# Performance work log

Measured on AMD Instinct MI355X. Metric: run time of the kernel, lower is better.

## Reference

```python
import jax, jax.numpy as jnp
import numpy as np

NUM_HEADS = 16
NUM_KV_HEADS = 8
HEAD_DIM = 256
HIDDEN = 2048
ROT_DIM = 64          # head_dim * partial_rotary_factor (0.25)
RMS_EPS = 1e-6
ROPE_THETA = 10000.0
SEQ = 2048


def _rmsnorm(x, weight=None):
    # Gemma RMSNorm: x * rsqrt(mean(x^2)+eps) * (1 + w); v_norm has no scale.
    var = jnp.mean(jnp.square(x), axis=-1, keepdims=True)
    n = x * jax.lax.rsqrt(var + RMS_EPS)
    if weight is not None:
        n = n * (1.0 + weight)
    return n


def _rope(x, positions):
    # Partial neox-style RoPE on the first ROT_DIM dims of each head.
    # x: [S, H, D]
    rot, rest = x[..., :ROT_DIM], x[..., ROT_DIM:]
    half = ROT_DIM // 2
    inv_freq = 1.0 / (ROPE_THETA ** (jnp.arange(0, ROT_DIM, 2, dtype=jnp.float32) / ROT_DIM))
    freqs = positions.astype(jnp.float32)[:, None] * inv_freq  # [S, half]
    cos = jnp.cos(freqs)[:, None, :]  # [S, 1, half]
    sin = jnp.sin(freqs)[:, None, :]
    x1, x2 = rot[..., :half], rot[..., half:]
    rot_out = jnp.concatenate([x1 * cos - x2 * sin, x2 * cos + x1 * sin], axis=-1)
    return jnp.concatenate([rot_out, rest], axis=-1)


def setup_inputs() -> dict:
    key = jax.random.key(0)
    k1, k2, k3, k4, k5 = jax.random.split(key, 5)
    q_size = NUM_HEADS * HEAD_DIM
    kv_size = NUM_KV_HEADS * HEAD_DIM
    return {
        "positions": jnp.arange(SEQ, dtype=jnp.int32),
        "hidden_states": jax.random.normal(k1, (SEQ, HIDDEN), dtype=jnp.float32),
        "w_qkv": jax.random.normal(k2, (q_size + 2 * kv_size, HIDDEN), dtype=jnp.float32) * (HIDDEN ** -0.5),
        "q_norm_w": jax.random.normal(k3, (HEAD_DIM,), dtype=jnp.float32) * 0.02,
        "k_norm_w": jax.random.normal(k4, (HEAD_DIM,), dtype=jnp.float32) * 0.02,
        "w_o": jax.random.normal(k5, (HIDDEN, q_size), dtype=jnp.float32) * (q_size ** -0.5),
    }


def reference(positions, hidden_states, w_qkv, q_norm_w, k_norm_w, w_o):
    S = hidden_states.shape[0]
    q_size = NUM_HEADS * HEAD_DIM
    kv_size = NUM_KV_HEADS * HEAD_DIM

    qkv = hidden_states @ w_qkv.T  # [S, q+2kv]
    q, k, v = jnp.split(qkv, [q_size, q_size + kv_size], axis=-1)
    q = q.reshape(S, NUM_HEADS, HEAD_DIM)
    k = k.reshape(S, NUM_KV_HEADS, HEAD_DIM)
    v = v.reshape(S, NUM_KV_HEADS, HEAD_DIM)

    # per-head RMSNorms (v_norm: scale_shift=0, with_scale=False -> pure norm)
    q = _rmsnorm(q, q_norm_w)
    k = _rmsnorm(k, k_norm_w)
    v = _rmsnorm(v, None)

    q = _rope(q, positions)
    k = _rope(k, positions)

    # GQA: repeat kv heads to match query heads
    rep = NUM_HEADS // NUM_KV_HEADS
    k = jnp.repeat(k, rep, axis=1)  # [S, H, D]
    v = jnp.repeat(v, rep, axis=1)

    # RadixAttention constructed with scaling=1.0 -> no 1/sqrt(d) scale
    scores = jnp.einsum("qhd,khd->hqk", q, k)  # [H, S, S]
    causal = positions[:, None] >= positions[None, :]  # [S, S]
    scores = jnp.where(causal[None, :, :], scores, jnp.float32(-1e30))
    attn = jax.nn.softmax(scores, axis=-1)
    out = jnp.einsum("hqk,khd->qhd", attn, v)  # [S, H, D]
    out = out.reshape(S, q_size)
    return out @ w_o.T  # [S, HIDDEN]
```

## Files before the change

kernel.cpp:

```cpp
#include <hip/hip_runtime.h>
#include <stdint.h>
#include <math.h>

#define SEQ 2048
#define HID 2048
#define NH 16
#define NKV 8
#define HD 256
#define QSZ 4096
#define QKVN 8192

typedef __attribute__((ext_vector_type(4))) float f32x4;
typedef _Float16 f16x8 __attribute__((ext_vector_type(8)));
typedef unsigned short u16;

__device__ __forceinline__ u16 f2h(float f) {
  _Float16 h = (_Float16)f;
  return __builtin_bit_cast(u16, h);
}
__device__ __forceinline__ float h2f(u16 b) {
  return (float)__builtin_bit_cast(_Float16, b);
}
__device__ __forceinline__ void glds16(const void* g, void* l) {
  __builtin_amdgcn_global_load_lds(
      (const __attribute__((address_space(1))) uint32_t*)g,
      (__attribute__((address_space(3))) uint32_t*)l, 16, 0, 0);
}

__global__ void cvt_f32_f16(const float* __restrict__ in, u16* __restrict__ out, int n4) {
  int i = blockIdx.x * 256 + threadIdx.x;
  if (i < n4) {
    float4 v = reinterpret_cast<const float4*>(in)[i];
    ushort4 o = make_ushort4(f2h(v.x), f2h(v.y), f2h(v.z), f2h(v.w));
    reinterpret_cast<ushort4*>(out)[i] = o;
  }
}

template <int F16OUT>
__global__ __launch_bounds__(256, 2) void gemm_bt(
    const u16* __restrict__ A, const u16* __restrict__ B, void* __restrict__ Cv,
    int M, int N, int K) {
  __shared__ __align__(16) u16 As[128 * 32];
  __shared__ __align__(16) u16 Bs[128 * 32];
  const int t = threadIdx.x;
  const int w = t >> 6, l = t & 63;
  const int bm = blockIdx.y * 128, bn = blockIdx.x * 128;
  const int wr = (w >> 1) * 64, wc = (w & 1) * 64;
  f32x4 acc[4][4] = {};

  const int arow = t >> 2;
  const int acol = (t & 3) * 8;
  const u16* Ag0 = A + (size_t)(bm + arow) * K + acol;
  const u16* Ag1 = A + (size_t)(bm + 64 + arow) * K + acol;
  const u16* Bg0 = B + (size_t)(bn + arow) * K + acol;
  const u16* Bg1 = B + (size_t)(bn + 64 + arow) * K + acol;
  u16* Al0 = As + w * 512;
  u16* Al1 = As + 2048 + w * 512;
  u16* Bl0 = Bs + w * 512;
  u16* Bl1 = Bs + 2048 + w * 512;

  const int lr = l & 15;
  const int lko = (l >> 4) * 8;

  for (int k0 = 0; k0 < K; k0 += 32) {
    __syncthreads();
    glds16(Ag0 + k0, Al0);
    glds16(Ag1 + k0, Al1);
    glds16(Bg0 + k0, Bl0);
    glds16(Bg1 + k0, Bl1);
    __syncthreads();
    f16x8 a[4], b[4];
#pragma unroll
    for (int m = 0; m < 4; ++m) a[m] = *(const f16x8*)&As[(wr + m * 16 + lr) * 32 + lko];
#pragma unroll
    for (int n = 0; n < 4; ++n) b[n] = *(const f16x8*)&Bs[(wc + n * 16 + lr) * 32 + lko];
#pragma unroll
    for (int m = 0; m < 4; ++m)
#pragma unroll
      for (int n = 0; n < 4; ++n)
        acc[m][n] = __builtin_amdgcn_mfma_f32_16x16x32_f16(a[m], b[n], acc[m][n], 0, 0, 0);
  }

#pragma unroll
  for (int m = 0; m < 4; ++m) {
#pragma unroll
    for (int n = 0; n < 4; ++n) {
      const int col = bn + wc + n * 16 + lr;
      const int row0 = bm + wr + m * 16 + (l >> 4) * 4;
#pragma unroll
      for (int j = 0; j < 4; ++j) {
        float vv = acc[m][n][j];
        if constexpr (F16OUT)
          ((u16*)Cv)[(size_t)(row0 + j) * N + col] = f2h(vv);
        else
          ((float*)Cv)[(size_t)(row0 + j) * N + col] = vv;
      }
    }
  }
}

__global__ void norm_rope(const u16* __restrict__ qkv, const float* __restrict__ qw,
                          const float* __restrict__ kw, const int* __restrict__ pos,
                          u16* __restrict__ qo, u16* __restrict__ ko, u16* __restrict__ vt) {
  const int b = blockIdx.x;
  const int s = b >> 5;
  const int slot = b & 31;
  const int l = threadIdx.x;
  const u16* row = qkv + (size_t)s * QKVN + slot * HD;
  ushort4 rv = *reinterpret_cast<const ushort4*>(row + l * 4);
  float x0 = h2f(rv.x), x1 = h2f(rv.y), x2 = h2f(rv.z), x3 = h2f(rv.w);
  float ss = x0 * x0 + x1 * x1 + x2 * x2 + x3 * x3;
#pragma unroll
  for (int mk = 32; mk; mk >>= 1) ss += __shfl_xor(ss, mk);
  const float rs = rsqrtf(ss * (1.0f / 256.0f) + 1e-6f);
  float n0, n1, n2, n3;
  if (slot < 16) {
    float4 wv = *reinterpret_cast<const float4*>(qw + l * 4);
    n0 = x0 * rs * (1.f + wv.x); n1 = x1 * rs * (1.f + wv.y);
    n2 = x2 * rs * (1.f + wv.z); n3 = x3 * rs * (1.f + wv.w);
  } else if (slot < 24) {
    float4 wv = *reinterpret_cast<const float4*>(kw + l * 4);
    n0 = x0 * rs * (1.f + wv.x); n1 = x1 * rs * (1.f + wv.y);
    n2 = x2 * rs * (1.f + wv.z); n3 = x3 * rs * (1.f + wv.w);
  } else {
    n0 = x0 * rs; n1 = x1 * rs; n2 = x2 * rs; n3 = x3 * rs;
  }
  if (slot < 24) {
    float p0 = __shfl_xor(n0, 8), p1 = __shfl_xor(n1, 8);
    float p2 = __shfl_xor(n2, 8), p3 = __shfl_xor(n3, 8);
    if (l < 16) {
      const double posd = (double)pos[s];
      float v[4] = {n0, n1, n2, n3};
      const float par[4] = {p0, p1, p2, p3};
#pragma unroll
      for (int i = 0; i < 4; ++i) {
        const int d = l * 4 + i;
        const int fi = d & 31;
        double inv = exp2(-(double)fi * (13.287712379549449 / 32.0));
        double ph = posd * inv;
        double tr = ph * 0.15915494309189535;
        tr -= floor(tr);
        float ang = (float)(tr * 6.283185307179586);
        float sn, cs;
        sincosf(ang, &sn, &cs);
        v[i] = (d < 32) ? (v[i] * cs - par[i] * sn) : (v[i] * cs + par[i] * sn);
      }
      n0 = v[0]; n1 = v[1]; n2 = v[2]; n3 = v[3];
    }
  }
  if (slot < 16) {
    ushort4 o = make_ushort4(f2h(n0), f2h(n1), f2h(n2), f2h(n3));
    *reinterpret_cast<ushort4*>(qo + ((size_t)slot * SEQ + s) * HD + l * 4) = o;
  } else if (slot < 24) {
    ushort4 o = make_ushort4(f2h(n0), f2h(n1), f2h(n2), f2h(n3));
    *reinterpret_cast<ushort4*>(ko + ((size_t)(slot - 16) * SEQ + s) * HD + l * 4) = o;
  } else {
    u16* base = vt + (size_t)(slot - 24) * HD * SEQ + s;
    base[(size_t)(l * 4 + 0) * SEQ] = f2h(n0);
    base[(size_t)(l * 4 + 1) * SEQ] = f2h(n1);
    base[(size_t)(l * 4 + 2) * SEQ] = f2h(n2);
    base[(size_t)(l * 4 + 3) * SEQ] = f2h(n3);
  }
}

__global__ __launch_bounds__(256, 2) void attn_fwd(
    const u16* __restrict__ Q, const u16* __restrict__ Kb,
    const u16* __restrict__ Vt, u16* __restrict__ O) {
  __shared__ __align__(16) u16 Ks[64 * 256];
  __shared__ __align__(16) u16 Vs[256 * 64];
  __shared__ __align__(16) u16 Ps[4 * 16 * 72];
  const int t = threadIdx.x, w = t >> 6, l = t & 63;
  const int bq = (gridDim.x - 1) - blockIdx.x;
  const int h = blockIdx.y;
  const int hk = h >> 1;
  const int lr = l & 15, lg = l >> 4;

  const u16* qrow = Q + ((size_t)h * SEQ + bq * 64 + w * 16 + lr) * HD + lg * 8;
  f16x8 qf[8];
#pragma unroll
  for (int c = 0; c < 8; ++c) qf[c] = *(const f16x8*)(qrow + c * 32);

  float m[4], lsum[4];
#pragma unroll
  for (int j = 0; j < 4; ++j) { m[j] = -1e30f; lsum[j] = 0.f; }
  f32x4 oacc[16] = {};

  const int krow_i = t >> 5;
  const int kchunk = t & 31;
  const int vrow_i = t >> 3;
  const int vchunk = t & 7;
  const u16* Kg = Kb + (size_t)hk * SEQ * HD;
  const u16* Vg = Vt + (size_t)hk * HD * SEQ;

  const int nt = bq + 1;
  for (int tt = 0; tt < nt; ++tt) {
    const int kv0 = tt * 64;
    __syncthreads();
#pragma unroll
    for (int i = 0; i < 8; ++i) {
      int row = i * 8 + krow_i;
      int sc = kchunk ^ (row & 7);
      glds16(Kg + (size_t)(kv0 + row) * HD + sc * 8, Ks + i * 2048 + w * 512);
    }
#pragma unroll
    for (int i = 0; i < 8; ++i) {
      int d = i * 32 + vrow_i;
      int sc = vchunk ^ (d & 7);
      glds16(Vg + (size_t)d * SEQ + kv0 + sc * 8, Vs + i * 2048 + w * 512);
    }
    __syncthreads();

    f32x4 sv[4];
#pragma unroll
    for (int n = 0; n < 4; ++n) {
      f32x4 s = {};
      const int krow = n * 16 + lr;
      const int rb = krow * 256;
      const int sw = krow & 7;
#pragma unroll
      for (int c = 0; c < 8; ++c) {
        const int chunk = (c * 4 + lg) ^ sw;
        f16x8 kf = *(const f16x8*)&Ks[rb + chunk * 8];
        s = __builtin_amdgcn_mfma_f32_16x16x32_f16(qf[c], kf, s, 0, 0, 0);
      }
      sv[n] = s;
    }
    const int qrow0 = bq * 64 + w * 16 + lg * 4;
#pragma unroll
    for (int n = 0; n < 4; ++n) {
      const int col = kv0 + n * 16 + lr;
#pragma unroll
      for (int j = 0; j < 4; ++j)
        if (col > qrow0 + j) sv[n][j] = -1e30f;
    }
    float pvv[4][4];
#pragma unroll
    for (int j = 0; j < 4; ++j) {
      float mx = fmaxf(fmaxf(sv[0][j], sv[1][j]), fmaxf(sv[2][j], sv[3][j]));
#pragma unroll
      for (int mk = 8; mk; mk >>= 1) mx = fmaxf(mx, __shfl_xor(mx, mk));
      const float mnew = fmaxf(m[j], mx);
      const float scale = __expf(m[j] - mnew);
      float rsum = 0.f;
#pragma unroll
      for (int n = 0; n < 4; ++n) {
        float e = __expf(sv[n][j] - mnew);
        pvv[n][j] = e;
        rsum += e;
      }
#pragma unroll
      for (int mk = 8; mk; mk >>= 1) rsum += __shfl_xor(rsum, mk);
      lsum[j] = lsum[j] * scale + rsum;
      m[j] = mnew;
#pragma unroll
      for (int nc = 0; nc < 16; ++nc) oacc[nc][j] *= scale;
    }
    u16* pb = Ps + w * 1152;
#pragma unroll
    for (int n = 0; n < 4; ++n)
#pragma unroll
      for (int j = 0; j < 4; ++j)
        pb[(lg * 4 + j) * 72 + n * 16 + lr] = f2h(pvv[n][j]);
#pragma unroll
    for (int kk = 0; kk < 2; ++kk) {
      f16x8 pa = *(const f16x8*)&pb[lr * 72 + kk * 32 + lg * 8];
#pragma unroll
      for (int nc = 0; nc < 16; ++nc) {
        const int drow = nc * 16 + lr;
        const int chunk = (kk * 4 + lg) ^ (drow & 7);
        f16x8 vf = *(const f16x8*)&Vs[drow * 64 + chunk * 8];
        oacc[nc] = __builtin_amdgcn_mfma_f32_16x16x32_f16(pa, vf, oacc[nc], 0, 0, 0);
      }
    }
  }
  float rl[4];
#pragma unroll
  for (int j = 0; j < 4; ++j) rl[j] = __fdividef(1.f, lsum[j]);
#pragma unroll
  for (int nc = 0; nc < 16; ++nc) {
#pragma unroll
    for (int j = 0; j < 4; ++j) {
      const int qr = bq * 64 + w * 16 + lg * 4 + j;
      O[(size_t)qr * QSZ + h * HD + nc * 16 + lr] = f2h(oacc[nc][j] * rl[j]);
    }
  }
}

extern "C" void kernel_launch(void* const* d_in, const int* in_sizes, int n_in,
                              void* d_out, int out_size, void* d_ws, size_t ws_size,
                              hipStream_t stream) {
  const int* pos = (const int*)d_in[0];
  const float* hidden = (const float*)d_in[1];
  const float* wqkv = (const float*)d_in[2];
  const float* qw = (const float*)d_in[3];
  const float* kw = (const float*)d_in[4];
  const float* wo_f = (const float*)d_in[5];
  float* out = (float*)d_out;

  char* wsp = (char*)d_ws;
  u16* hb = (u16*)(wsp);
  u16* wqb = (u16*)(wsp + (8ll << 20));
  u16* wob = (u16*)(wsp + (40ll << 20));
  u16* qkvb = (u16*)(wsp + (56ll << 20));
  u16* qb = (u16*)(wsp);
  u16* kb = (u16*)(wsp + (16ll << 20));
  u16* vt = (u16*)(wsp + (24ll << 20));
  u16* ao = (u16*)(wsp + (56ll << 20));

  cvt_f32_f16<<<(HID * HID / 4 + 255) / 256, 256, 0, stream>>>(hidden, hb, HID * HID / 4);
  cvt_f32_f16<<<(QKVN * HID / 4 + 255) / 256, 256, 0, stream>>>(wqkv, wqb, QKVN * HID / 4);
  cvt_f32_f16<<<(HID * QSZ / 4 + 255) / 256, 256, 0, stream>>>(wo_f, wob, HID * QSZ / 4);

  gemm_bt<1><<<dim3(QKVN / 128, SEQ / 128), 256, 0, stream>>>(hb, wqb, (void*)qkvb, SEQ, QKVN, HID);
  norm_rope<<<SEQ * 32, 64, 0, stream>>>(qkvb, qw, kw, pos, qb, kb, vt);
  attn_fwd<<<dim3(SEQ / 64, NH), 256, 0, stream>>>(qb, kb, vt, ao);
  gemm_bt<0><<<dim3(HID / 128, SEQ / 128), 256, 0, stream>>>(ao, wob, (void*)out, SEQ, HID, QSZ);
}
```

Measured before the change: 362.0 us.

## Double-buffer K/V tiles in attention and add lazy softmax rescaling

The attention kernel now keeps two LDS buffers for K and V. It issues the global-to-LDS loads for the next tile before computing on the current one, so there is one barrier per iteration instead of two. Causal masking is skipped for tiles that lie entirely below the diagonal. The online-softmax rescale of the accumulators and running sum now runs only when the row max grows by more than a threshold. Doubling LDS use forces launch bounds down to one block per CU, which lowers occupancy and the latency hiding that came from running two blocks per CU.

```diff
diff --git a/kernel.cpp b/kernel.cpp
--- a/kernel.cpp
+++ b/kernel.cpp
@@ -163,11 +163,11 @@
   }
 }
 
-__global__ __launch_bounds__(256, 2) void attn_fwd(
+__global__ __launch_bounds__(256, 1) void attn_fwd(
     const u16* __restrict__ Q, const u16* __restrict__ Kb,
     const u16* __restrict__ Vt, u16* __restrict__ O) {
-  __shared__ __align__(16) u16 Ks[64 * 256];
-  __shared__ __align__(16) u16 Vs[256 * 64];
+  __shared__ __align__(16) u16 Ks[2][64 * 256];
+  __shared__ __align__(16) u16 Vs[2][256 * 64];
   __shared__ __align__(16) u16 Ps[4 * 16 * 72];
   const int t = threadIdx.x, w = t >> 6, l = t & 63;
   const int bq = (gridDim.x - 1) - blockIdx.x;
@@ -192,23 +192,33 @@
   const u16* Kg = Kb + (size_t)hk * SEQ * HD;
   const u16* Vg = Vt + (size_t)hk * HD * SEQ;
 
-  const int nt = bq + 1;
-  for (int tt = 0; tt < nt; ++tt) {
+  auto STAGE = [&](int tt, int buf) {
     const int kv0 = tt * 64;
-    __syncthreads();
 #pragma unroll
     for (int i = 0; i < 8; ++i) {
       int row = i * 8 + krow_i;
       int sc = kchunk ^ (row & 7);
-      glds16(Kg + (size_t)(kv0 + row) * HD + sc * 8, Ks + i * 2048 + w * 512);
+      glds16(Kg + (size_t)(kv0 + row) * HD + sc * 8, &Ks[buf][i * 2048 + w * 512]);
     }
 #pragma unroll
     for (int i = 0; i < 8; ++i) {
       int d = i * 32 + vrow_i;
       int sc = vchunk ^ (d & 7);
-      glds16(Vg + (size_t)d * SEQ + kv0 + sc * 8, Vs + i * 2048 + w * 512);
-    }
-    __syncthreads();
+      glds16(Vg + (size_t)d * SEQ + kv0 + sc * 8, &Vs[buf][i * 2048 + w * 512]);
+    }
+  };
+
+  const int nt = bq + 1;
+  STAGE(0, 0);
+  __syncthreads();
+  int cur = 0;
+
+  for (int tt = 0; tt < nt; ++tt) {
+    if (tt + 1 < nt) STAGE(tt + 1, cur ^ 1);
+
+    const int kv0 = tt * 64;
+    const u16* Kc = &Ks[cur][0];
+    const u16* Vc = &Vs[cur][0];
 
     f32x4 sv[4];
 #pragma unroll
@@ -220,18 +230,20 @@
 #pragma unroll
       for (int c = 0; c < 8; ++c) {
         const int chunk = (c * 4 + lg) ^ sw;
-        f16x8 kf = *(const f16x8*)&Ks[rb + chunk * 8];
+        f16x8 kf = *(const f16x8*)&Kc[rb + chunk * 8];
         s = __builtin_amdgcn_mfma_f32_16x16x32_f16(qf[c], kf, s, 0, 0, 0);
       }
       sv[n] = s;
     }
     const int qrow0 = bq * 64 + w * 16 + lg * 4;
-#pragma unroll
-    for (int n = 0; n < 4; ++n) {
-      const int col = kv0 + n * 16 + lr;
-#pragma unroll
-      for (int j = 0; j < 4; ++j)
-        if (col > qrow0 + j) sv[n][j] = -1e30f;
+    if (kv0 + 63 > bq * 64 + w * 16) {
+#pragma unroll
+      for (int n = 0; n < 4; ++n) {
+        const int col = kv0 + n * 16 + lr;
+#pragma unroll
+        for (int j = 0; j < 4; ++j)
+          if (col > qrow0 + j) sv[n][j] = -1e30f;
+      }
     }
     float pvv[4][4];
 #pragma unroll
@@ -239,21 +251,23 @@
       float mx = fmaxf(fmaxf(sv[0][j], sv[1][j]), fmaxf(sv[2][j], sv[3][j]));
 #pragma unroll
       for (int mk = 8; mk; mk >>= 1) mx = fmaxf(mx, __shfl_xor(mx, mk));
-      const float mnew = fmaxf(m[j], mx);
-      const float scale = __expf(m[j] - mnew);
+      if (mx > m[j] + 8.f) {
+        const float scale = __expf(m[j] - mx);
+        m[j] = mx;
+        lsum[j] *= scale;
+#pragma unroll
+        for (int nc = 0; nc < 16; ++nc) oacc[nc][j] *= scale;
+      }
       float rsum = 0.f;
 #pragma unroll
       for (int n = 0; n < 4; ++n) {
-        float e = __expf(sv[n][j] - mnew);
+        float e = __expf(sv[n][j] - m[j]);
         pvv[n][j] = e;
         rsum += e;
       }
 #pragma unroll
       for (int mk = 8; mk; mk >>= 1) rsum += __shfl_xor(rsum, mk);
-      lsum[j] = lsum[j] * scale + rsum;
-      m[j] = mnew;
-#pragma unroll
-      for (int nc = 0; nc < 16; ++nc) oacc[nc][j] *= scale;
+      lsum[j] += rsum;
     }
     u16* pb = Ps + w * 1152;
 #pragma unroll
@@ -268,10 +282,12 @@
       for (int nc = 0; nc < 16; ++nc) {
         const int drow = nc * 16 + lr;
         const int chunk = (kk * 4 + lg) ^ (drow & 7);
-        f16x8 vf = *(const f16x8*)&Vs[drow * 64 + chunk * 8];
+        f16x8 vf = *(const f16x8*)&Vc[drow * 64 + chunk * 8];
         oacc[nc] = __builtin_amdgcn_mfma_f32_16x16x32_f16(pa, vf, oacc[nc], 0, 0, 0);
       }
     }
+    __syncthreads();
+    cur ^= 1;
   }
   float rl[4];
 #pragma unroll
```

After: 468.4 us. +29.4%, slower.
